# Optimization experiments

Hardware: AMD Instinct MI355X
Metric: run time of the kernel (lower is better)

## Reference

```python
import jax, jax.numpy as jnp
import numpy as np

DIM_SED = 256
DIM_DOA = 256
DIM_ATTN = 256
NUM_HEADS = 8
HEAD_DIM = DIM_ATTN // NUM_HEADS
SCALE = HEAD_DIM ** -0.5
B, N_SED, N_DOA = 2, 2048, 2048


def setup_inputs() -> dict:
    key = jax.random.key(0)
    ks = jax.random.split(key, 8)
    s = lambda fan_in: 1.0 / np.sqrt(fan_in)
    return {
        "x_sed": jax.random.normal(ks[0], (B, N_SED, DIM_SED), jnp.float32),
        "x_doa": jax.random.normal(ks[1], (B, N_DOA, DIM_DOA), jnp.float32),
        # nn.Linear stores weight as [out, in]; we keep [in, out] for x @ W
        "W_sed_in": jax.random.uniform(ks[2], (DIM_SED, 2 * DIM_ATTN), jnp.float32, -s(DIM_SED), s(DIM_SED)),
        "W_doa_in": jax.random.uniform(ks[3], (DIM_DOA, 2 * DIM_ATTN), jnp.float32, -s(DIM_DOA), s(DIM_DOA)),
        "W_sed_out": jax.random.uniform(ks[4], (DIM_ATTN, DIM_SED), jnp.float32, -s(DIM_ATTN), s(DIM_ATTN)),
        "b_sed_out": jax.random.uniform(ks[5], (DIM_SED,), jnp.float32, -s(DIM_ATTN), s(DIM_ATTN)),
        "W_doa_out": jax.random.uniform(ks[6], (DIM_ATTN, DIM_DOA), jnp.float32, -s(DIM_ATTN), s(DIM_ATTN)),
        "b_doa_out": jax.random.uniform(ks[7], (DIM_DOA,), jnp.float32, -s(DIM_ATTN), s(DIM_ATTN)),
    }


def _split_heads(rv, B, N):
    # rv: [B, N, 2*DIM_ATTN] -> r, v each [B, H, N, hd]
    rv = rv.reshape(B, N, 2, NUM_HEADS, HEAD_DIM).transpose(2, 0, 3, 1, 4)
    return rv[0], rv[1]


def reference(x_sed, x_doa, W_sed_in, W_doa_in, W_sed_out, b_sed_out, W_doa_out, b_doa_out):
    B_, Ns, _ = x_sed.shape
    _, Nd, _ = x_doa.shape
    r_sed, v_sed = _split_heads(x_sed @ W_sed_in, B_, Ns)  # [B,H,Ns,hd]
    r_doa, v_doa = _split_heads(x_doa @ W_doa_in, B_, Nd)  # [B,H,Nd,hd]

    # Shared score matrix, softmaxed in both directions (dropout = identity, eval mode)
    attn = jnp.einsum('bhsd,bhtd->bhst', r_sed, r_doa) * SCALE  # [B,H,Ns,Nd]
    attn_sed2doa = jax.nn.softmax(attn, axis=-1)               # row-wise
    attn_doa2sed = jax.nn.softmax(attn, axis=-2)               # col-wise (softmax of attn^T over last dim)

    x_sed_fused = jnp.einsum('bhst,bhtd->bhsd', attn_sed2doa, v_doa)
    x_sed_fused = x_sed_fused.transpose(0, 2, 1, 3).reshape(B_, Ns, DIM_ATTN)
    x_sed_fused = x_sed_fused @ W_sed_out + b_sed_out

    x_doa_fused = jnp.einsum('bhst,bhsd->bhtd', attn_doa2sed, v_sed)
    x_doa_fused = x_doa_fused.transpose(0, 2, 1, 3).reshape(B_, Nd, DIM_ATTN)
    x_doa_fused = x_doa_fused @ W_doa_out + b_doa_out
    return (x_sed_fused, x_doa_fused)
```

## Files before the change

kernel.cpp:

```cpp
#include <hip/hip_runtime.h>
#include <hip/hip_bf16.h>

typedef short short8 __attribute__((ext_vector_type(8)));
typedef float f32x4 __attribute__((ext_vector_type(4)));
typedef float f32x16 __attribute__((ext_vector_type(16)));
typedef unsigned int uint4v __attribute__((ext_vector_type(4)));
typedef unsigned short ushort_t;

__device__ inline ushort_t f2bf(float f) {
    union { float f; unsigned u; } x; x.f = f;
    unsigned r = x.u + 0x7fffu + ((x.u >> 16) & 1u);
    return (ushort_t)(r >> 16);
}
__device__ inline ushort_t f2bf_u(float x) {
    union { __hip_bfloat16 h; ushort_t u; } cv;
    cv.h = __float2bfloat16(x);
    return cv.u;
}
__device__ inline float bf2f(ushort_t u) {
    union { unsigned u; float f; } cv; cv.u = ((unsigned)u) << 16; return cv.f;
}

#define GLD_LDS16(src, dst)                                                  \
    __builtin_amdgcn_global_load_lds(                                        \
        (const __attribute__((address_space(1))) void*)(src),                \
        (__attribute__((address_space(3))) void*)(dst), 16, 0, 0)

#define RSQ 0.5050100f

__global__ __launch_bounds__(256) void prep_w_kernel(const float* __restrict__ w0,
                                                     const float* __restrict__ w1,
                                                     const float* __restrict__ w2,
                                                     const float* __restrict__ w3,
                                                     ushort_t* __restrict__ t0,
                                                     ushort_t* __restrict__ t1,
                                                     ushort_t* __restrict__ t2,
                                                     ushort_t* __restrict__ t3) {
    __shared__ float tile[64][65];
    int z = blockIdx.y;
    const float* W; ushort_t* T; int J;
    if (z == 0)      { W = w0; T = t0; J = 512; }
    else if (z == 1) { W = w1; T = t1; J = 512; }
    else if (z == 2) { W = w2; T = t2; J = 256; }
    else             { W = w3; T = t3; J = 256; }
    int ntj = J >> 6;
    int nt = ntj * 4;
    int tix = blockIdx.x;
    if (tix >= nt) return;
    int tj = tix % ntj, tk = tix / ntj;
    int j0 = tj * 64, k0 = tk * 64;
    int tid = threadIdx.x;

    int jj = (tid & 15) * 4, kk0 = tid >> 4;
    #pragma unroll
    for (int kk = kk0; kk < 64; kk += 16) {
        float4 v = *reinterpret_cast<const float4*>(&W[(size_t)(k0 + kk) * J + j0 + jj]);
        tile[kk][jj] = v.x; tile[kk][jj + 1] = v.y;
        tile[kk][jj + 2] = v.z; tile[kk][jj + 3] = v.w;
    }
    __syncthreads();
    int kk4 = (tid & 15) * 4, jj0 = tid >> 4;
    #pragma unroll
    for (int j2 = jj0; j2 < 64; j2 += 16) {
        ushort4 o;
        o.x = f2bf(tile[kk4][j2]);     o.y = f2bf(tile[kk4 + 1][j2]);
        o.z = f2bf(tile[kk4 + 2][j2]); o.w = f2bf(tile[kk4 + 3][j2]);
        *reinterpret_cast<ushort4*>(&T[(size_t)(j0 + j2) * 256 + k0 + kk4]) = o;
    }
}

__global__ __launch_bounds__(256) void gemm_in_kernel(
    const float* __restrict__ A0, const float* __restrict__ A1,
    const ushort_t* __restrict__ B0, const ushort_t* __restrict__ B1,
    ushort_t* __restrict__ R0, ushort_t* __restrict__ R1,
    ushort_t* __restrict__ V0, ushort_t* __restrict__ V1) {
    const float* A = blockIdx.z ? A1 : A0;
    const ushort_t* Bt = blockIdx.z ? B1 : B0;
    ushort_t* R = blockIdx.z ? R1 : R0;
    ushort_t* Vt = blockIdx.z ? V1 : V0;
    constexpr int K = 256;
    const int w = threadIdx.x >> 6, lane = threadIdx.x & 63;
    const int l16 = lane & 15, g = lane >> 4;
    const int m0 = blockIdx.x * 64 + w * 16;
    const int cb = blockIdx.y * 128;

    f32x4 acc[8] = {};
    const float* Ap = A + (size_t)(m0 + l16) * K + 8 * g;
    const ushort_t* Bp = Bt + (size_t)(cb + l16) * K + 8 * g;

    #pragma unroll
    for (int ks = 0; ks < K; ks += 32) {
        float4 af0 = *reinterpret_cast<const float4*>(Ap + ks);
        float4 af1 = *reinterpret_cast<const float4*>(Ap + ks + 4);
        short8 a;
        a[0] = (short)f2bf_u(af0.x); a[1] = (short)f2bf_u(af0.y);
        a[2] = (short)f2bf_u(af0.z); a[3] = (short)f2bf_u(af0.w);
        a[4] = (short)f2bf_u(af1.x); a[5] = (short)f2bf_u(af1.y);
        a[6] = (short)f2bf_u(af1.z); a[7] = (short)f2bf_u(af1.w);
        #pragma unroll
        for (int c = 0; c < 8; ++c) {
            short8 b = *reinterpret_cast<const short8*>(Bp + (size_t)c * 16 * K + ks);
            acc[c] = __builtin_amdgcn_mfma_f32_16x16x32_bf16(a, b, acc[c], 0, 0, 0);
        }
    }

    if (blockIdx.y < 2) {
        #pragma unroll
        for (int c = 0; c < 8; ++c) {
            int col = cb + c * 16 + l16;
            int h = col >> 5, d = col & 31;
            #pragma unroll
            for (int r = 0; r < 4; ++r) {
                int row = m0 + 4 * g + r;
                int bb = row >> 11, n = row & 2047;
                size_t base = (size_t)(bb * 8 + h) * 65536;
                int unit = ((n >> 5) * 4 + (d >> 4) * 2 + ((d >> 3) & 1)) * 32 + (n & 31);
                R[base + (size_t)unit * 8 + (d & 7)] = f2bf_u(acc[c][r] * RSQ);
            }
        }
    } else {
        #pragma unroll
        for (int c = 0; c < 8; ++c) {
            int colp = cb - 256 + c * 16 + l16;
            int h = colp >> 5, d = colp & 31;
            int row = m0 + 4 * g;
            int bb = row >> 11, n = row & 2047;
            size_t base = (size_t)(bb * 8 + h) * 65536;
            int nl = n & 31;
            int vh = nl >> 4, r4 = nl & 15;
            int hi2 = (r4 >> 2) & 1;
            int e0 = (r4 & 3) + 4 * (r4 >> 3);
            int unit = ((n >> 5) * 4 + vh * 2 + hi2) * 32 + d;
            ushort4 s;
            s.x = f2bf_u(acc[c][0]); s.y = f2bf_u(acc[c][1]);
            s.z = f2bf_u(acc[c][2]); s.w = f2bf_u(acc[c][3]);
            *reinterpret_cast<ushort4*>(Vt + base + (size_t)unit * 8 + e0) = s;
        }
    }
}

__global__ __launch_bounds__(256, 5) void attn_kernel(
    const ushort_t* __restrict__ rU_sed, const ushort_t* __restrict__ rU_doa,
    const ushort_t* __restrict__ vU_sed, const ushort_t* __restrict__ vU_doa,
    ushort_t* __restrict__ part,
    float* __restrict__ lpart) {
    __shared__ __align__(16) ushort_t smem[16384];

    const int bid = blockIdx.x;
    const int xcd = bid & 7, i = bid >> 3;
    const int stream = xcd * 4 + (i & 3);
    const int rest = i >> 2;
    const int qblk = rest & 15, kvq = rest >> 4;
    const int dir = stream >> 4, bh = stream & 15;

    const ushort_t* rQ = dir ? rU_doa : rU_sed;
    const ushort_t* rK = dir ? rU_sed : rU_doa;
    const ushort_t* vV = dir ? vU_sed : vU_doa;

    const int tid = threadIdx.x;
    const int w = tid >> 6, lane = tid & 63;
    const int l31 = lane & 31, hi = lane >> 5;
    const size_t sB = (size_t)bh * 65536;
    const int qbase = qblk * 128 + w * 32;

    const short8 qf0 = *reinterpret_cast<const short8*>(rQ + sB + (size_t)qbase * 32 + lane * 8);
    const short8 qf1 = *reinterpret_cast<const short8*>(rQ + sB + (size_t)qbase * 32 + 512 + lane * 8);

    const ushort_t* Kbase = rK + sB + (size_t)kvq * 16384;
    const ushort_t* Vbase = vV + sB + (size_t)kvq * 16384;
    const ushort_t* srcK = Kbase + tid * 8;
    const ushort_t* srcV = Vbase + tid * 8;

    f32x16 acc = {};
    f32x4 lv = {};

    auto stage = [&](int t, int bufsel) {
        const ushort_t* sk = srcK + (size_t)t * 4096;
        const ushort_t* sv = srcV + (size_t)t * 4096;
        ushort_t* dk = &smem[bufsel * 8192 + w * 512];
        GLD_LDS16(sk,        dk);
        GLD_LDS16(sk + 2048, dk + 2048);
        GLD_LDS16(sv,        dk + 4096);
        GLD_LDS16(sv + 2048, dk + 6144);
    };

    int buf = 0;
    stage(0, 0);
    __syncthreads();

    for (int t = 0; t < 4; ++t) {
        if (t < 3) stage(t + 1, buf ^ 1);
        const ushort_t* KB = &smem[buf * 8192];
        const ushort_t* VB = KB + 4096;
        #pragma unroll
        for (int s = 0; s < 4; ++s) {
            short8 kf0 = *reinterpret_cast<const short8*>(KB + s * 1024 + lane * 8);
            short8 kf1 = *reinterpret_cast<const short8*>(KB + s * 1024 + 512 + lane * 8);
            short8 vf0 = *reinterpret_cast<const short8*>(VB + s * 1024 + lane * 8);
            short8 vf1 = *reinterpret_cast<const short8*>(VB + s * 1024 + 512 + lane * 8);

            f32x16 z16 = {};
            f32x16 st = __builtin_amdgcn_mfma_f32_32x32x16_bf16(kf0, qf0, z16, 0, 0, 0);
            st = __builtin_amdgcn_mfma_f32_32x32x16_bf16(kf1, qf1, st, 0, 0, 0);

            short8 c1s, c2s;
            {
                float p[8]; unsigned pk[4];
                #pragma unroll
                for (int j = 0; j < 8; ++j) p[j] = __builtin_amdgcn_exp2f(st[j]);
                #pragma unroll
                for (int j = 0; j < 8; ++j) lv[j & 3] += p[j];
                #pragma unroll
                for (int j = 0; j < 4; ++j) {
                    asm("v_cvt_pk_bf16_f32 %0, %1, %2" : "=v"(pk[j]) : "v"(p[2 * j]), "v"(p[2 * j + 1]));
                }
                union { uint4v u; short8 s; } cc;
                cc.u = uint4v{pk[0], pk[1], pk[2], pk[3]};
                c1s = cc.s;
            }
            {
                float p[8]; unsigned pk[4];
                #pragma unroll
                for (int j = 0; j < 8; ++j) p[j] = __builtin_amdgcn_exp2f(st[8 + j]);
                #pragma unroll
                for (int j = 0; j < 8; ++j) lv[j & 3] += p[j];
                #pragma unroll
                for (int j = 0; j < 4; ++j) {
                    asm("v_cvt_pk_bf16_f32 %0, %1, %2" : "=v"(pk[j]) : "v"(p[2 * j]), "v"(p[2 * j + 1]));
                }
                union { uint4v u; short8 s; } cc;
                cc.u = uint4v{pk[0], pk[1], pk[2], pk[3]};
                c2s = cc.s;
            }

            acc = __builtin_amdgcn_mfma_f32_32x32x16_bf16(vf0, c1s, acc, 0, 0, 0);
            acc = __builtin_amdgcn_mfma_f32_32x32x16_bf16(vf1, c2s, acc, 0, 0, 0);
        }
        __syncthreads();
        buf ^= 1;
    }

    float l = (lv[0] + lv[1]) + (lv[2] + lv[3]);
    l += __shfl_xor(l, 32);
    const int q = qbase + l31;
    const size_t prow = ((size_t)stream * 4 + kvq) * 2048 + q;
    if (lane < 32) lpart[prow] = l;
    ushort_t* pa = part + prow * 32;
    #pragma unroll
    for (int r = 0; r < 16; ++r) {
        int d = (r & 3) + 8 * (r >> 2) + 4 * hi;
        pa[d] = f2bf(acc[r]);
    }
}

__global__ __launch_bounds__(256) void gemm_out_kernel(
    const ushort_t* __restrict__ part, const float* __restrict__ lpart,
    const ushort_t* __restrict__ b0, const ushort_t* __restrict__ b1,
    float* __restrict__ c0, float* __restrict__ c1,
    const float* __restrict__ bias0, const float* __restrict__ bias1) {
    const int z = blockIdx.z;
    const ushort_t* Bt = z ? b1 : b0;
    float* C = z ? c1 : c0;
    const float* bias = z ? bias1 : bias0;
    constexpr int K = 256, N = 256;
    const int w = threadIdx.x >> 6, lane = threadIdx.x & 63;
    const int l16 = lane & 15, g = lane >> 4;
    const int m0 = blockIdx.x * 64 + w * 16;
    const int cb = blockIdx.y * 128;

    const int row = m0 + l16;
    const int bb = row >> 11, q = row & 2047;

    f32x4 acc[8] = {};
    const ushort_t* Bp = Bt + (size_t)(cb + l16) * K + 8 * g;
    #pragma unroll
    for (int it = 0; it < 8; ++it) {
        const int strm = z * 16 + bb * 8 + it;
        const size_t pr0 = ((size_t)strm * 4) * 2048 + q;
        float l = lpart[pr0] + lpart[pr0 + 2048] + lpart[pr0 + 4096] + lpart[pr0 + 6144];
        float inv = 1.0f / l;
        const ushort_t* p0 = part + pr0 * 32 + 8 * g;
        short8 pa = *reinterpret_cast<const short8*>(p0);
        short8 pb = *reinterpret_cast<const short8*>(p0 + (size_t)2048 * 32);
        short8 pc = *reinterpret_cast<const short8*>(p0 + (size_t)4096 * 32);
        short8 pd = *reinterpret_cast<const short8*>(p0 + (size_t)6144 * 32);
        short8 a;
        #pragma unroll
        for (int e = 0; e < 8; ++e) {
            float sum = (bf2f((ushort_t)pa[e]) + bf2f((ushort_t)pb[e]))
                      + (bf2f((ushort_t)pc[e]) + bf2f((ushort_t)pd[e]));
            a[e] = (short)f2bf_u(sum * inv);
        }
        #pragma unroll
        for (int c = 0; c < 8; ++c) {
            short8 b = *reinterpret_cast<const short8*>(Bp + (size_t)c * 16 * K + it * 32);
            acc[c] = __builtin_amdgcn_mfma_f32_16x16x32_bf16(a, b, acc[c], 0, 0, 0);
        }
    }
    #pragma unroll
    for (int c = 0; c < 8; ++c) {
        int col = cb + c * 16 + l16;
        #pragma unroll
        for (int r = 0; r < 4; ++r) {
            int orow = m0 + 4 * g + r;
            C[(size_t)orow * N + col] = acc[c][r] + bias[col];
        }
    }
}

extern "C" void kernel_launch(void* const* d_in, const int* in_sizes, int n_in,
                              void* d_out, int out_size, void* d_ws, size_t ws_size,
                              hipStream_t stream) {
    const float* x_sed     = (const float*)d_in[0];
    const float* x_doa     = (const float*)d_in[1];
    const float* W_sed_in  = (const float*)d_in[2];
    const float* W_doa_in  = (const float*)d_in[3];
    const float* W_sed_out = (const float*)d_in[4];
    const float* b_sed_out = (const float*)d_in[5];
    const float* W_doa_out = (const float*)d_in[6];
    const float* b_doa_out = (const float*)d_in[7];
    float* out = (float*)d_out;

    ushort_t* ws = (ushort_t*)d_ws;
    ushort_t* wt_si  = ws;
    ushort_t* wt_di  = wt_si  + 131072;
    ushort_t* wt_so  = wt_di  + 131072;
    ushort_t* wt_do  = wt_so  + 65536;
    ushort_t* rU_sed = wt_do  + 65536;
    ushort_t* rU_doa = rU_sed + 1048576;
    ushort_t* vU_sed = rU_doa + 1048576;
    ushort_t* vU_doa = vU_sed + 1048576;
    ushort_t* part   = vU_doa + 1048576;
    float*    lpart  = (float*)(part + 8388608);

    prep_w_kernel<<<dim3(32, 4), 256, 0, stream>>>(W_sed_in, W_doa_in, W_sed_out, W_doa_out,
                                                   wt_si, wt_di, wt_so, wt_do);
    gemm_in_kernel<<<dim3(64, 4, 2), 256, 0, stream>>>(x_sed, x_doa, wt_si, wt_di,
                                                       rU_sed, rU_doa, vU_sed, vU_doa);
    attn_kernel<<<dim3(2048), 256, 0, stream>>>(rU_sed, rU_doa, vU_sed, vU_doa, part, lpart);
    gemm_out_kernel<<<dim3(64, 2, 2), 256, 0, stream>>>(part, lpart, wt_so, wt_do,
                                                        out, out + 1048576, b_sed_out, b_doa_out);
}
```

Baseline: 68.17 us.

## Replace exp2 with Schraudolph bit-trick and compute row sums via MFMA

Inside the attention kernel, each exp2 is replaced by a Schraudolph-style approximation: an fma into the bf16 exponent bits, a float-to-int conversion and a byte permute that packs pairs directly into bf16. The per-row softmax denominators now come from extra MFMAs against a ones vector instead of VALU adds and a shuffle. This moves work from the transcendental and VALU units onto the matrix cores. The trade-off is lower accuracy in the exponentials, two more MFMAs per step, and an occupancy hint lowered from 5 to 4. The projection kernel also swaps scalar bf16 conversions for packed v_cvt_pk_bf16_f32.

```diff
diff --git a/kernel.cpp b/kernel.cpp
--- a/kernel.cpp
+++ b/kernel.cpp
@@ -27,6 +27,7 @@
         (__attribute__((address_space(3))) void*)(dst), 16, 0, 0)
 
 #define RSQ 0.5050100f
+#define SCHRA_C 16252.02f
 
 __global__ __launch_bounds__(256) void prep_w_kernel(const float* __restrict__ w0,
                                                      const float* __restrict__ w1,
@@ -92,11 +93,14 @@
     for (int ks = 0; ks < K; ks += 32) {
         float4 af0 = *reinterpret_cast<const float4*>(Ap + ks);
         float4 af1 = *reinterpret_cast<const float4*>(Ap + ks + 4);
-        short8 a;
-        a[0] = (short)f2bf_u(af0.x); a[1] = (short)f2bf_u(af0.y);
-        a[2] = (short)f2bf_u(af0.z); a[3] = (short)f2bf_u(af0.w);
-        a[4] = (short)f2bf_u(af1.x); a[5] = (short)f2bf_u(af1.y);
-        a[6] = (short)f2bf_u(af1.z); a[7] = (short)f2bf_u(af1.w);
+        unsigned pk0, pk1, pk2, pk3;
+        asm("v_cvt_pk_bf16_f32 %0, %1, %2" : "=v"(pk0) : "v"(af0.x), "v"(af0.y));
+        asm("v_cvt_pk_bf16_f32 %0, %1, %2" : "=v"(pk1) : "v"(af0.z), "v"(af0.w));
+        asm("v_cvt_pk_bf16_f32 %0, %1, %2" : "=v"(pk2) : "v"(af1.x), "v"(af1.y));
+        asm("v_cvt_pk_bf16_f32 %0, %1, %2" : "=v"(pk3) : "v"(af1.z), "v"(af1.w));
+        union { uint4v u; short8 s; } ua;
+        ua.u = uint4v{pk0, pk1, pk2, pk3};
+        short8 a = ua.s;
         #pragma unroll
         for (int c = 0; c < 8; ++c) {
             short8 b = *reinterpret_cast<const short8*>(Bp + (size_t)c * 16 * K + ks);
@@ -131,15 +135,17 @@
             int hi2 = (r4 >> 2) & 1;
             int e0 = (r4 & 3) + 4 * (r4 >> 3);
             int unit = ((n >> 5) * 4 + vh * 2 + hi2) * 32 + d;
-            ushort4 s;
-            s.x = f2bf_u(acc[c][0]); s.y = f2bf_u(acc[c][1]);
-            s.z = f2bf_u(acc[c][2]); s.w = f2bf_u(acc[c][3]);
-            *reinterpret_cast<ushort4*>(Vt + base + (size_t)unit * 8 + e0) = s;
-        }
-    }
-}
-
-__global__ __launch_bounds__(256, 5) void attn_kernel(
+            unsigned w0p, w1p;
+            asm("v_cvt_pk_bf16_f32 %0, %1, %2" : "=v"(w0p) : "v"(acc[c][0]), "v"(acc[c][1]));
+            asm("v_cvt_pk_bf16_f32 %0, %1, %2" : "=v"(w1p) : "v"(acc[c][2]), "v"(acc[c][3]));
+            union { unsigned u[2]; ushort4 s; } us;
+            us.u[0] = w0p; us.u[1] = w1p;
+            *reinterpret_cast<ushort4*>(Vt + base + (size_t)unit * 8 + e0) = us.s;
+        }
+    }
+}
+
+__global__ __launch_bounds__(256, 4) void attn_kernel(
     const ushort_t* __restrict__ rU_sed, const ushort_t* __restrict__ rU_doa,
     const ushort_t* __restrict__ vU_sed, const ushort_t* __restrict__ vU_doa,
     ushort_t* __restrict__ part,
@@ -171,8 +177,12 @@
     const ushort_t* srcK = Kbase + tid * 8;
     const ushort_t* srcV = Vbase + tid * 8;
 
+    short8 ones8;
+    #pragma unroll
+    for (int j = 0; j < 8; ++j) ones8[j] = (short)0x3F80;
+
     f32x16 acc = {};
-    f32x4 lv = {};
+    f32x16 lacc = {};
 
     auto stage = [&](int t, int bufsel) {
         const ushort_t* sk = srcK + (size_t)t * 4096;
@@ -205,46 +215,38 @@
 
             short8 c1s, c2s;
             {
-                float p[8]; unsigned pk[4];
+                int u[8];
                 #pragma unroll
-                for (int j = 0; j < 8; ++j) p[j] = __builtin_amdgcn_exp2f(st[j]);
+                for (int j = 0; j < 8; ++j) u[j] = (int)__builtin_fmaf(st[j], 128.0f, SCHRA_C);
+                union { uint4v uu; short8 s; } cc;
                 #pragma unroll
-                for (int j = 0; j < 8; ++j) lv[j & 3] += p[j];
-                #pragma unroll
-                for (int j = 0; j < 4; ++j) {
-                    asm("v_cvt_pk_bf16_f32 %0, %1, %2" : "=v"(pk[j]) : "v"(p[2 * j]), "v"(p[2 * j + 1]));
-                }
-                union { uint4v u; short8 s; } cc;
-                cc.u = uint4v{pk[0], pk[1], pk[2], pk[3]};
+                for (int j = 0; j < 4; ++j)
+                    cc.uu[j] = __builtin_amdgcn_perm((unsigned)u[2 * j + 1], (unsigned)u[2 * j], 0x05040100u);
                 c1s = cc.s;
             }
             {
-                float p[8]; unsigned pk[4];
+                int u[8];
                 #pragma unroll
-                for (int j = 0; j < 8; ++j) p[j] = __builtin_amdgcn_exp2f(st[8 + j]);
+                for (int j = 0; j < 8; ++j) u[j] = (int)__builtin_fmaf(st[8 + j], 128.0f, SCHRA_C);
+                union { uint4v uu; short8 s; } cc;
                 #pragma unroll
-                for (int j = 0; j < 8; ++j) lv[j & 3] += p[j];
-                #pragma unroll
-                for (int j = 0; j < 4; ++j) {
-                    asm("v_cvt_pk_bf16_f32 %0, %1, %2" : "=v"(pk[j]) : "v"(p[2 * j]), "v"(p[2 * j + 1]));
-                }
-                union { uint4v u; short8 s; } cc;
-                cc.u = uint4v{pk[0], pk[1], pk[2], pk[3]};
+                for (int j = 0; j < 4; ++j)
+                    cc.uu[j] = __builtin_amdgcn_perm((unsigned)u[2 * j + 1], (unsigned)u[2 * j], 0x05040100u);
                 c2s = cc.s;
             }
 
             acc = __builtin_amdgcn_mfma_f32_32x32x16_bf16(vf0, c1s, acc, 0, 0, 0);
             acc = __builtin_amdgcn_mfma_f32_32x32x16_bf16(vf1, c2s, acc, 0, 0, 0);
+            lacc = __builtin_amdgcn_mfma_f32_32x32x16_bf16(ones8, c1s, lacc, 0, 0, 0);
+            lacc = __builtin_amdgcn_mfma_f32_32x32x16_bf16(ones8, c2s, lacc, 0, 0, 0);
         }
         __syncthreads();
         buf ^= 1;
     }
 
-    float l = (lv[0] + lv[1]) + (lv[2] + lv[3]);
-    l += __shfl_xor(l, 32);
     const int q = qbase + l31;
     const size_t prow = ((size_t)stream * 4 + kvq) * 2048 + q;
-    if (lane < 32) lpart[prow] = l;
+    if (lane < 32) lpart[prow] = lacc[0];
     ushort_t* pa = part + prow * 32;
     #pragma unroll
     for (int r = 0; r < 16; ++r) {
```

New measurement: 69.06 us. No clear change (+1.3%).
